# Kernel optimization log

Measured on AMD Instinct MI355X. Metric: run time of the kernel, lower is better.

## Reference

```python
import jax, jax.numpy as jnp
import numpy as np

C = 128  # in_dim

def _proj(x, w, b):
    # 1x1 conv: x [b,c,h,w], w [out,in], b [out] -> [b,out,h*w]
    bsz, c, h, wd = x.shape
    y = jnp.einsum('bchw,oc->bohw', x, w) + b[None, :, None, None]
    return y.reshape(bsz, -1, h * wd)

def setup_inputs() -> dict:
    key = jax.random.key(0)
    ks = jax.random.split(key, 7)
    x = jax.random.normal(ks[0], (16, C, 128, 128), dtype=jnp.float32)
    s = 1.0 / np.sqrt(C)
    qw = jax.random.normal(ks[1], (C, C), dtype=jnp.float32) * s
    kw = jax.random.normal(ks[2], (C, C), dtype=jnp.float32) * s
    vw = jax.random.normal(ks[3], (C, C), dtype=jnp.float32) * s
    qb = jax.random.normal(ks[4], (C,), dtype=jnp.float32) * 0.01
    kb = jax.random.normal(ks[5], (C,), dtype=jnp.float32) * 0.01
    vb = jax.random.normal(ks[6], (C,), dtype=jnp.float32) * 0.01
    return {'x': x, 'qw': qw, 'qb': qb, 'kw': kw, 'kb': kb, 'vw': vw, 'vb': vb}

def reference(x, qw, qb, kw, kb, vw, vb):
    x_s, x_t = jnp.split(x, 2, axis=0)
    b, c, h, w = x_s.shape
    q_s = _proj(x_s, qw, qb); q_t = _proj(x_t, qw, qb)   # [b,c,N]
    k_s = _proj(x_s, kw, kb); k_t = _proj(x_t, kw, kb)   # [b,c,N]
    v_s = _proj(x_s, vw, vb); v_t = _proj(x_t, vw, vb)   # [b,c,N]
    # channel cross-attentions: contract over spatial N -> [b,c,c]
    a_st = jax.nn.softmax(jnp.einsum('bcn,bdn->bcd', q_t, k_s), axis=-1)
    a_ts = jax.nn.softmax(jnp.einsum('bcn,bdn->bcd', q_s, k_t), axis=-1)
    att = jax.nn.softmax(jnp.einsum('bce,bde->bcd', a_st, a_ts), axis=-1)
    out_s = jnp.einsum('bcd,bdn->bcn', att, v_s).reshape(b, c, h, w)
    out_t = jnp.einsum('bcd,bdn->bcn', att, v_t).reshape(b, c, h, w)
    return jnp.concatenate((x_s + out_s, x_t + out_t), axis=0)
```

## Files before the change

### kernel.cpp

```cpp
#include <hip/hip_runtime.h>
#include <hip/hip_bf16.h>

#define CC 128
#define NSP 16384
#define NFULL (CC * NSP)

typedef float f32x4 __attribute__((ext_vector_type(4)));
typedef short s16x8 __attribute__((ext_vector_type(8)));
typedef unsigned int u32x4 __attribute__((ext_vector_type(4)));

__device__ __forceinline__ unsigned bf16rne(float f) {
  unsigned u = __float_as_uint(f);
  return ((u + 0x7FFFu + ((u >> 16) & 1u)) >> 16) & 0xFFFFu;
}

__device__ __forceinline__ uint2 packpair(float x0, float x1) {
  __hip_bfloat162 h2 = __float22bfloat162_rn(make_float2(x0, x1));
  unsigned hu = *reinterpret_cast<unsigned*>(&h2);
  float hf0 = __uint_as_float(hu << 16);
  float hf1 = __uint_as_float(hu & 0xFFFF0000u);
  __hip_bfloat162 l2 = __float22bfloat162_rn(make_float2(x0 - hf0, x1 - hf1));
  unsigned lu = *reinterpret_cast<unsigned*>(&l2);
  return make_uint2(hu, lu);
}

__global__ __launch_bounds__(256) void zerok(float* __restrict__ p, int n) {
  int i = blockIdx.x * 256 + threadIdx.x;
  if (i < n) p[i] = 0.f;
}

__global__ __launch_bounds__(256, 2) void k1_mfma(const float* __restrict__ x,
    float* __restrict__ Mdst, float* __restrict__ rs, float* __restrict__ rt,
    float* __restrict__ rspart, float* __restrict__ rtpart,
    int nst, int mode) {
  const int b = blockIdx.y;
  const int chunk = blockIdx.x;
  const int n0 = chunk * (nst * 64);
  const int t = threadIdx.x;
  const int w = t >> 6, l = t & 63;
  const int wr = w >> 1, wc = w & 1;
  const int lr = l & 15, lg = l >> 4;
  const int r0 = t >> 2;
  const int q = t & 3;
  __shared__ unsigned short Ahi[128 * 64];
  __shared__ unsigned short Alo[128 * 64];
  __shared__ unsigned short Bhi[128 * 64];
  __shared__ unsigned short Blo[128 * 64];
  const float* Xs = x + (size_t)b * NFULL;
  const float* Xt = x + (size_t)(b + 8) * NFULL;

  f32x4 acc[4][4];
#pragma unroll
  for (int a = 0; a < 4; ++a)
#pragma unroll
    for (int bb = 0; bb < 4; ++bb) acc[a][bb] = (f32x4){0.f, 0.f, 0.f, 0.f};
  float rtp[2] = {0.f, 0.f}, rsp[2] = {0.f, 0.f};

  for (int s = 0; s < nst; ++s) {
    const int nb = n0 + s * 64;
    __syncthreads();
#pragma unroll
    for (int p = 0; p < 2; ++p) {
      const int row = r0 + 64 * p;
      const float* At = Xt + (size_t)row * NSP + nb + q * 16;
      const float* Bs = Xs + (size_t)row * NSP + nb + q * 16;
      f32x4 av[4], bv[4];
#pragma unroll
      for (int i = 0; i < 4; ++i) av[i] = *(const f32x4*)(At + i * 4);
#pragma unroll
      for (int i = 0; i < 4; ++i) bv[i] = *(const f32x4*)(Bs + i * 4);
#pragma unroll
      for (int i = 0; i < 4; ++i) {
        rtp[p] += (av[i][0] + av[i][1]) + (av[i][2] + av[i][3]);
        rsp[p] += (bv[i][0] + bv[i][1]) + (bv[i][2] + bv[i][3]);
      }
      u32x4 h0, l0, h1, l1;
#pragma unroll
      for (int i = 0; i < 2; ++i) {
        uint2 r1 = packpair(av[i][0], av[i][1]);
        h0[2 * i] = r1.x; l0[2 * i] = r1.y;
        uint2 r2 = packpair(av[i][2], av[i][3]);
        h0[2 * i + 1] = r2.x; l0[2 * i + 1] = r2.y;
        uint2 r3 = packpair(av[2 + i][0], av[2 + i][1]);
        h1[2 * i] = r3.x; l1[2 * i] = r3.y;
        uint2 r4 = packpair(av[2 + i][2], av[2 + i][3]);
        h1[2 * i + 1] = r4.x; l1[2 * i + 1] = r4.y;
      }
      {
        int base = row * 128 + q * 32;
        int sw = (row & 7) << 4;
        *(u32x4*)((char*)Ahi + ((base) ^ sw)) = h0;
        *(u32x4*)((char*)Ahi + ((base + 16) ^ sw)) = h1;
        *(u32x4*)((char*)Alo + ((base) ^ sw)) = l0;
        *(u32x4*)((char*)Alo + ((base + 16) ^ sw)) = l1;
      }
#pragma unroll
      for (int i = 0; i < 2; ++i) {
        uint2 r1 = packpair(bv[i][0], bv[i][1]);
        h0[2 * i] = r1.x; l0[2 * i] = r1.y;
        uint2 r2 = packpair(bv[i][2], bv[i][3]);
        h0[2 * i + 1] = r2.x; l0[2 * i + 1] = r2.y;
        uint2 r3 = packpair(bv[2 + i][0], bv[2 + i][1]);
        h1[2 * i] = r3.x; l1[2 * i] = r3.y;
        uint2 r4 = packpair(bv[2 + i][2], bv[2 + i][3]);
        h1[2 * i + 1] = r4.x; l1[2 * i + 1] = r4.y;
      }
      {
        int base = row * 128 + q * 32;
        int sw = (row & 7) << 4;
        *(u32x4*)((char*)Bhi + ((base) ^ sw)) = h0;
        *(u32x4*)((char*)Bhi + ((base + 16) ^ sw)) = h1;
        *(u32x4*)((char*)Blo + ((base) ^ sw)) = l0;
        *(u32x4*)((char*)Blo + ((base + 16) ^ sw)) = l1;
      }
    }
    __syncthreads();
#pragma unroll
    for (int kk = 0; kk < 2; ++kk) {
      s16x8 ah[4], al[4], bh[4], bl[4];
#pragma unroll
      for (int a = 0; a < 4; ++a) {
        int row = wr * 64 + a * 16 + lr;
        int off = (row * 128 + kk * 64 + lg * 16) ^ ((row & 7) << 4);
        ah[a] = *(const s16x8*)((char*)Ahi + off);
        al[a] = *(const s16x8*)((char*)Alo + off);
      }
#pragma unroll
      for (int bb = 0; bb < 4; ++bb) {
        int row = wc * 64 + bb * 16 + lr;
        int off = (row * 128 + kk * 64 + lg * 16) ^ ((row & 7) << 4);
        bh[bb] = *(const s16x8*)((char*)Bhi + off);
        bl[bb] = *(const s16x8*)((char*)Blo + off);
      }
#pragma unroll
      for (int a = 0; a < 4; ++a)
#pragma unroll
        for (int bb = 0; bb < 4; ++bb) {
          acc[a][bb] = __builtin_amdgcn_mfma_f32_16x16x32_bf16(ah[a], bh[bb], acc[a][bb], 0, 0, 0);
          acc[a][bb] = __builtin_amdgcn_mfma_f32_16x16x32_bf16(ah[a], bl[bb], acc[a][bb], 0, 0, 0);
          acc[a][bb] = __builtin_amdgcn_mfma_f32_16x16x32_bf16(al[a], bh[bb], acc[a][bb], 0, 0, 0);
        }
    }
  }

#pragma unroll
  for (int p = 0; p < 2; ++p) {
    float vt = rtp[p];
    vt += __shfl_xor(vt, 1);
    vt += __shfl_xor(vt, 2);
    float vs = rsp[p];
    vs += __shfl_xor(vs, 1);
    vs += __shfl_xor(vs, 2);
    if (q == 0) {
      int row = r0 + 64 * p;
      if (mode == 0) {
        rtpart[((size_t)chunk * 8 + b) * CC + row] = vt;
        rspart[((size_t)chunk * 8 + b) * CC + row] = vs;
      } else {
        atomicAdd(&rt[b * CC + row], vt);
        atomicAdd(&rs[b * CC + row], vs);
      }
    }
  }

  const int rquad = lg << 2;
  if (mode == 0) {
    float* Mp = Mdst + ((size_t)chunk * 8 + b) * (CC * CC);
#pragma unroll
    for (int a = 0; a < 4; ++a)
#pragma unroll
      for (int bb = 0; bb < 4; ++bb)
#pragma unroll
        for (int r = 0; r < 4; ++r) {
          int i = wr * 64 + a * 16 + rquad + r;
          int j = wc * 64 + bb * 16 + lr;
          Mp[i * CC + j] = acc[a][bb][r];
        }
  } else {
    float* Mp = Mdst + (size_t)b * (CC * CC);
#pragma unroll
    for (int a = 0; a < 4; ++a)
#pragma unroll
      for (int bb = 0; bb < 4; ++bb)
#pragma unroll
        for (int r = 0; r < 4; ++r) {
          int i = wr * 64 + a * 16 + rquad + r;
          int j = wc * 64 + bb * 16 + lr;
          atomicAdd(&Mp[i * CC + j], acc[a][bb][r]);
        }
  }
}

__global__ __launch_bounds__(256) void k1_reduce(const float* __restrict__ Mpart,
    const float* __restrict__ rspart, const float* __restrict__ rtpart,
    float* __restrict__ M, float* __restrict__ rs, float* __restrict__ rt,
    int NB) {
  const int t = threadIdx.x;
  if (blockIdx.x < 128) {
    const int i4 = blockIdx.x * 256 + t;
    const int b = i4 >> 12;
    const int e = (i4 & 4095) * 4;
    f32x4 s = (f32x4){0.f, 0.f, 0.f, 0.f};
    for (int c = 0; c < NB; ++c) {
      f32x4 v = *(const f32x4*)(Mpart + ((size_t)c * 8 + b) * (CC * CC) + e);
      s += v;
    }
    *(f32x4*)(M + (size_t)b * CC * CC + e) = s;
  } else if (blockIdx.x == 128) {
    const int e = t * 4;
    f32x4 s = (f32x4){0.f, 0.f, 0.f, 0.f};
    for (int c = 0; c < NB; ++c) s += *(const f32x4*)(rtpart + (size_t)c * 1024 + e);
    *(f32x4*)(rt + e) = s;
  } else {
    const int e = t * 4;
    f32x4 s = (f32x4){0.f, 0.f, 0.f, 0.f};
    for (int c = 0; c < NB; ++c) s += *(const f32x4*)(rspart + (size_t)c * 1024 + e);
    *(f32x4*)(rs + e) = s;
  }
}

__global__ __launch_bounds__(256) void k2ab(const float* __restrict__ M,
    const float* __restrict__ qw, const float* __restrict__ kw,
    const float* __restrict__ qb, const float* __restrict__ kb,
    const float* __restrict__ rs, const float* __restrict__ rt,
    float* __restrict__ Ast, float* __restrict__ Ats) {
  const int b = blockIdx.y;
  const int c0 = blockIdx.x * 8;
  __shared__ float Big[128][132];
  __shared__ float Wq[8][128];
  __shared__ float T12[2][8][128];
  __shared__ float uvv[2][8];
  __shared__ float wv2[2][128];
  const int t = threadIdx.x;
  const float* Mb = M + (size_t)b * CC * CC;
#pragma unroll
  for (int p = 0; p < 16; ++p) {
    int f = p * 256 + t;
    int row = f >> 5, c4 = (f & 31) * 4;
    *(f32x4*)&Big[row][c4] = *(const f32x4*)(Mb + row * CC + c4);
  }
  { int row = t >> 5, c4 = (t & 31) * 4;
    *(f32x4*)&Wq[row][c4] = *(const f32x4*)(qw + (c0 + row) * CC + c4); }
  __syncthreads();
  if (t < 16) {
    int c = t & 7;
    const float* r = ((t < 8) ? rs : rt) + b * CC;
    float s = 0.f;
    for (int i = 0; i < CC; ++i) s += Wq[c][i] * r[i];
    uvv[(t < 8) ? 1 : 0][c] = s;
  }
  const int tr = t >> 5;
  const int L = t & 31;
  {
    float a1[4] = {0.f, 0.f, 0.f, 0.f}, a2[4] = {0.f, 0.f, 0.f, 0.f};
    for (int i = 0; i < CC; ++i) {
      float wq = Wq[tr][i];
#pragma unroll
      for (int j = 0; j < 4; ++j) a1[j] += wq * Big[i][L + 32 * j];
    }
    for (int i4 = 0; i4 < 32; ++i4) {
      f32x4 wq4 = *(const f32x4*)&Wq[tr][i4 * 4];
#pragma unroll
      for (int j = 0; j < 4; ++j) {
        f32x4 m4 = *(const f32x4*)&Big[L + 32 * j][i4 * 4];
        a2[j] += wq4[0]*m4[0] + wq4[1]*m4[1] + wq4[2]*m4[2] + wq4[3]*m4[3];
      }
    }
#pragma unroll
    for (int j = 0; j < 4; ++j) {
      T12[0][tr][L + 32 * j] = a1[j];
      T12[1][tr][L + 32 * j] = a2[j];
    }
  }
  __syncthreads();
#pragma unroll
  for (int p = 0; p < 16; ++p) {
    int f = p * 256 + t;
    int row = f >> 5, c4 = (f & 31) * 4;
    *(f32x4*)&Big[row][c4] = *(const f32x4*)(kw + row * CC + c4);
  }
  __syncthreads();
  {
    int d = t & 127, wh = t >> 7;
    const float* r = (wh ? rt : rs) + b * CC;
    float s = 0.f;
    for (int i4 = 0; i4 < 32; ++i4) {
      f32x4 w4 = *(const f32x4*)&Big[d][i4 * 4];
      s += w4[0]*r[i4*4] + w4[1]*r[i4*4+1] + w4[2]*r[i4*4+2] + w4[3]*r[i4*4+3];
    }
    wv2[wh][d] = s;
  }
  __syncthreads();
  const int c = c0 + tr;
  const float bqc = qb[c];
#pragma unroll 1
  for (int which = 0; which < 2; ++which) {
    float g[4];
#pragma unroll
    for (int j = 0; j < 4; ++j) {
      int d = L + 32 * j;
      g[j] = uvv[which][tr] * kb[d] + bqc * wv2[which][d] + 16384.f * bqc * kb[d];
    }
    for (int j4 = 0; j4 < 32; ++j4) {
      f32x4 tv4 = *(const f32x4*)&T12[which][tr][j4 * 4];
#pragma unroll
      for (int j = 0; j < 4; ++j) {
        f32x4 w4 = *(const f32x4*)&Big[L + 32 * j][j4 * 4];
        g[j] += tv4[0]*w4[0] + tv4[1]*w4[1] + tv4[2]*w4[2] + tv4[3]*w4[3];
      }
    }
    float m = fmaxf(fmaxf(g[0], g[1]), fmaxf(g[2], g[3]));
#pragma unroll
    for (int off = 1; off < 32; off <<= 1) m = fmaxf(m, __shfl_xor(m, off));
    float s = 0.f;
#pragma unroll
    for (int j = 0; j < 4; ++j) { g[j] = expf(g[j] - m); s += g[j]; }
#pragma unroll
    for (int off = 1; off < 32; off <<= 1) s += __shfl_xor(s, off);
    const float inv = 1.f / s;
    float* A = (which ? Ats : Ast) + (size_t)b * CC * CC + (size_t)c * CC;
#pragma unroll
    for (int j = 0; j < 4; ++j) A[L + 32 * j] = g[j] * inv;
  }
}

__global__ __launch_bounds__(256) void k2cd(const float* __restrict__ Ast,
    const float* __restrict__ Ats, const float* __restrict__ vw,
    const float* __restrict__ vb, unsigned short* __restrict__ Pbf,
    float* __restrict__ c0v) {
  const int b = blockIdx.y;
  const int c0 = blockIdx.x * 8;
  __shared__ float Big[128][132];
  __shared__ float Tl[8][128];
  __shared__ float Al[8][128];
  const int t = threadIdx.x;
  const float* Bb = Ats + (size_t)b * CC * CC;
  const float* Tb = Ast + (size_t)b * CC * CC;
#pragma unroll
  for (int p = 0; p < 16; ++p) {
    int f = p * 256 + t;
    int row = f >> 5, c4 = (f & 31) * 4;
    *(f32x4*)&Big[row][c4] = *(const f32x4*)(Bb + row * CC + c4);
  }
  { int row = t >> 5, c4 = (t & 31) * 4;
    *(f32x4*)&Tl[row][c4] = *(const f32x4*)(Tb + (c0 + row) * CC + c4); }
  __syncthreads();
  const int tr = t >> 5;
  const int L = t & 31;
  {
    float g[4] = {0.f, 0.f, 0.f, 0.f};
    for (int e4 = 0; e4 < 32; ++e4) {
      f32x4 tv4 = *(const f32x4*)&Tl[tr][e4 * 4];
#pragma unroll
      for (int j = 0; j < 4; ++j) {
        f32x4 a4 = *(const f32x4*)&Big[L + 32 * j][e4 * 4];
        g[j] += tv4[0]*a4[0] + tv4[1]*a4[1] + tv4[2]*a4[2] + tv4[3]*a4[3];
      }
    }
    float m = fmaxf(fmaxf(g[0], g[1]), fmaxf(g[2], g[3]));
#pragma unroll
    for (int off = 1; off < 32; off <<= 1) m = fmaxf(m, __shfl_xor(m, off));
    float s = 0.f;
#pragma unroll
    for (int j = 0; j < 4; ++j) { g[j] = expf(g[j] - m); s += g[j]; }
#pragma unroll
    for (int off = 1; off < 32; off <<= 1) s += __shfl_xor(s, off);
    const float inv = 1.f / s;
#pragma unroll
    for (int j = 0; j < 4; ++j) Al[tr][L + 32 * j] = g[j] * inv;
  }
  __syncthreads();
#pragma unroll
  for (int p = 0; p < 16; ++p) {
    int f = p * 256 + t;
    int row = f >> 5, c4 = (f & 31) * 4;
    *(f32x4*)&Big[row][c4] = *(const f32x4*)(vw + row * CC + c4);
  }
  __syncthreads();
  float p4[4] = {0.f, 0.f, 0.f, 0.f};
  for (int d = 0; d < CC; ++d) {
    float av = Al[tr][d];
#pragma unroll
    for (int j = 0; j < 4; ++j) p4[j] += av * Big[d][L + 32 * j];
  }
  float csum = 0.f;
#pragma unroll
  for (int j = 0; j < 4; ++j) csum += Al[tr][L + 32 * j] * vb[L + 32 * j];
#pragma unroll
  for (int off = 1; off < 32; off <<= 1) csum += __shfl_xor(csum, off);
  const int c = c0 + tr;
  if ((c & 31) == L) p4[c >> 5] += 1.0f;
  unsigned short* Pp = Pbf + (size_t)b * CC * CC + (size_t)c * CC;
#pragma unroll
  for (int j = 0; j < 4; ++j) Pp[L + 32 * j] = (unsigned short)bf16rne(p4[j]);
  if (L == 0) c0v[b * CC + c] = csum;
}

__global__ __launch_bounds__(256, 2) void k3_mfma(const float* __restrict__ x,
    const unsigned short* __restrict__ Pbf, const float* __restrict__ c0v,
    float* __restrict__ out) {
  const int im = blockIdx.y;
  const int pb = im & 7;
  const int n0 = blockIdx.x * 256;
  const float* X = x + (size_t)im * NFULL;
  float* O = out + (size_t)im * NFULL;
  __shared__ unsigned short XT[256 * 128];
  __shared__ float c0l[128];
  const int t = threadIdx.x;
  if (t < 128) c0l[t] = c0v[pb * CC + t];
#pragma unroll
  for (int p = 0; p < 16; ++p) {
    int d0 = 2 * (t >> 4) + 32 * (p & 3);
    int n4 = (t & 15) * 4 + 64 * (p >> 2);
    f32x4 x0 = *(const f32x4*)(X + (size_t)d0 * NSP + n0 + n4);
    f32x4 x1 = *(const f32x4*)(X + (size_t)(d0 + 1) * NSP + n0 + n4);
#pragma unroll
    for (int i = 0; i < 4; ++i) {
      int n = n4 + i;
      __hip_bfloat162 h2 = __float22bfloat162_rn(make_float2(x0[i], x1[i]));
      unsigned pk = *reinterpret_cast<unsigned*>(&h2);
      int off = (n * 256 + d0 * 2) ^ (((n >> 2) & 15) << 4);
      *(unsigned*)((char*)XT + off) = pk;
    }
  }
  __syncthreads();

  const int w = t >> 6, l = t & 63;
  const int ln = l & 15, lg = l >> 4;
#pragma unroll
  for (int h = 0; h < 2; ++h) {
    const unsigned short* Pg = Pbf + (size_t)pb * (CC * CC)
                             + (size_t)(h * 64 + ln) * CC + lg * 8;
    s16x8 Af[4][4];
#pragma unroll
    for (int a = 0; a < 4; ++a)
#pragma unroll
      for (int kk = 0; kk < 4; ++kk)
        Af[a][kk] = *(const s16x8*)(Pg + a * 16 * CC + kk * 32);
#pragma unroll
    for (int sub = 0; sub < 4; ++sub) {
      int row = sub * 64 + w * 16 + ln;
      int sw = ((row >> 2) & 15) << 4;
      s16x8 bf[4];
#pragma unroll
      for (int kk = 0; kk < 4; ++kk)
        bf[kk] = *(const s16x8*)((char*)XT + ((row * 256 + kk * 64 + lg * 16) ^ sw));
      f32x4 acc[4];
#pragma unroll
      for (int a = 0; a < 4; ++a) acc[a] = (f32x4){0.f, 0.f, 0.f, 0.f};
#pragma unroll
      for (int kk = 0; kk < 4; ++kk)
#pragma unroll
        for (int a = 0; a < 4; ++a)
          acc[a] = __builtin_amdgcn_mfma_f32_16x16x32_bf16(Af[a][kk], bf[kk], acc[a], 0, 0, 0);
      int n = n0 + sub * 64 + w * 16 + ln;
#pragma unroll
      for (int a = 0; a < 4; ++a)
#pragma unroll
        for (int r = 0; r < 4; ++r) {
          int c = h * 64 + a * 16 + lg * 4 + r;
          __builtin_nontemporal_store(acc[a][r] + c0l[c], O + (size_t)c * NSP + n);
        }
    }
  }
}

extern "C" void kernel_launch(void* const* d_in, const int* in_sizes, int n_in,
                              void* d_out, int out_size, void* d_ws, size_t ws_size,
                              hipStream_t stream) {
  (void)in_sizes; (void)n_in; (void)out_size;
  const float* x  = (const float*)d_in[0];
  const float* qw = (const float*)d_in[1];
  const float* qb = (const float*)d_in[2];
  const float* kw = (const float*)d_in[3];
  const float* kb = (const float*)d_in[4];
  const float* vw = (const float*)d_in[5];
  const float* vb = (const float*)d_in[6];
  float* out = (float*)d_out;
  float* ws = (float*)d_ws;
  float* M   = ws;
  float* rs  = M + 131072;
  float* rt  = rs + 1024;
  float* AST = rt + 1024;
  float* ATS = AST + 131072;
  unsigned short* Pbf = (unsigned short*)(ATS + 131072);
  float* c0v = ATS + 131072 + 65536;
  float* Mpart = c0v + 1024;
  const size_t base_floats = (size_t)(Mpart - ws);

  int NB, mode;
  if (ws_size >= (base_floats + (size_t)64 * (131072 + 2048)) * 4) { NB = 64; mode = 0; }
  else if (ws_size >= (base_floats + (size_t)32 * (131072 + 2048)) * 4) { NB = 32; mode = 0; }
  else { NB = 32; mode = 1; }
  const int nst = (16384 / NB) / 64;
  float* rtpart = Mpart + (size_t)NB * 131072;
  float* rspart = rtpart + (size_t)NB * 1024;

  if (mode == 1) zerok<<<(133120 + 255) / 256, 256, 0, stream>>>(M, 133120);
  k1_mfma<<<dim3(NB, 8), 256, 0, stream>>>(x, mode ? M : Mpart, rs, rt,
                                           rspart, rtpart, nst, mode);
  if (mode == 0)
    k1_reduce<<<130, 256, 0, stream>>>(Mpart, rspart, rtpart, M, rs, rt, NB);
  k2ab<<<dim3(16, 8), 256, 0, stream>>>(M, qw, kw, qb, kb, rs, rt, AST, ATS);
  k2cd<<<dim3(16, 8), 256, 0, stream>>>(AST, ATS, vw, vb, Pbf, c0v);
  k3_mfma<<<dim3(64, 16), 256, 0, stream>>>(x, Pbf, c0v, out);
}
```

Measured before the change: 145.6 us.

## Double-buffer raw fp32 tiles via direct global-to-LDS loads and split at fragment read

Result: no change. 147.2 us (+1.1%).

```diff
diff --git a/kernel.cpp b/kernel.cpp
--- a/kernel.cpp
+++ b/kernel.cpp
@@ -8,6 +8,10 @@
 typedef float f32x4 __attribute__((ext_vector_type(4)));
 typedef short s16x8 __attribute__((ext_vector_type(8)));
 typedef unsigned int u32x4 __attribute__((ext_vector_type(4)));
+
+#define GLOAD16(g, l) __builtin_amdgcn_global_load_lds( \
+    (const __attribute__((address_space(1))) void*)(g), \
+    (__attribute__((address_space(3))) void*)(l), 16, 0, 0)
 
 __device__ __forceinline__ unsigned bf16rne(float f) {
   unsigned u = __float_as_uint(f);
@@ -35,130 +39,111 @@
     int nst, int mode) {
   const int b = blockIdx.y;
   const int chunk = blockIdx.x;
-  const int n0 = chunk * (nst * 64);
+  const int n0 = chunk * (nst * 32);
   const int t = threadIdx.x;
   const int w = t >> 6, l = t & 63;
   const int wr = w >> 1, wc = w & 1;
   const int lr = l & 15, lg = l >> 4;
-  const int r0 = t >> 2;
-  const int q = t & 3;
-  __shared__ unsigned short Ahi[128 * 64];
-  __shared__ unsigned short Alo[128 * 64];
-  __shared__ unsigned short Bhi[128 * 64];
-  __shared__ unsigned short Blo[128 * 64];
+  __shared__ __align__(16) char LB[2][2][128 * 128];
   const float* Xs = x + (size_t)b * NFULL;
   const float* Xt = x + (size_t)(b + 8) * NFULL;
+  const int srow0 = w * 32 + (l >> 3);
+  const int sn16x = (l & 7);
 
   f32x4 acc[4][4];
 #pragma unroll
   for (int a = 0; a < 4; ++a)
 #pragma unroll
     for (int bb = 0; bb < 4; ++bb) acc[a][bb] = (f32x4){0.f, 0.f, 0.f, 0.f};
-  float rtp[2] = {0.f, 0.f}, rsp[2] = {0.f, 0.f};
+  float rtp[4] = {0.f, 0.f, 0.f, 0.f};
+  float rsp[4] = {0.f, 0.f, 0.f, 0.f};
+
+  {
+#pragma unroll
+    for (int i = 0; i < 4; ++i) {
+      int row = srow0 + i * 8;
+      int n16 = sn16x ^ (row & 7);
+      GLOAD16(Xt + (size_t)row * NSP + n0 + n16 * 4, &LB[0][0][(w * 32 + i * 8) * 128]);
+      GLOAD16(Xs + (size_t)row * NSP + n0 + n16 * 4, &LB[0][1][(w * 32 + i * 8) * 128]);
+    }
+  }
 
   for (int s = 0; s < nst; ++s) {
-    const int nb = n0 + s * 64;
+    const int cur = s & 1;
     __syncthreads();
-#pragma unroll
-    for (int p = 0; p < 2; ++p) {
-      const int row = r0 + 64 * p;
-      const float* At = Xt + (size_t)row * NSP + nb + q * 16;
-      const float* Bs = Xs + (size_t)row * NSP + nb + q * 16;
-      f32x4 av[4], bv[4];
-#pragma unroll
-      for (int i = 0; i < 4; ++i) av[i] = *(const f32x4*)(At + i * 4);
-#pragma unroll
-      for (int i = 0; i < 4; ++i) bv[i] = *(const f32x4*)(Bs + i * 4);
+    if (s + 1 < nst) {
+      const int nb = n0 + (s + 1) * 32;
 #pragma unroll
       for (int i = 0; i < 4; ++i) {
-        rtp[p] += (av[i][0] + av[i][1]) + (av[i][2] + av[i][3]);
-        rsp[p] += (bv[i][0] + bv[i][1]) + (bv[i][2] + bv[i][3]);
-      }
-      u32x4 h0, l0, h1, l1;
-#pragma unroll
-      for (int i = 0; i < 2; ++i) {
-        uint2 r1 = packpair(av[i][0], av[i][1]);
-        h0[2 * i] = r1.x; l0[2 * i] = r1.y;
-        uint2 r2 = packpair(av[i][2], av[i][3]);
-        h0[2 * i + 1] = r2.x; l0[2 * i + 1] = r2.y;
-        uint2 r3 = packpair(av[2 + i][0], av[2 + i][1]);
-        h1[2 * i] = r3.x; l1[2 * i] = r3.y;
-        uint2 r4 = packpair(av[2 + i][2], av[2 + i][3]);
-        h1[2 * i + 1] = r4.x; l1[2 * i + 1] = r4.y;
-      }
-      {
-        int base = row * 128 + q * 32;
-        int sw = (row & 7) << 4;
-        *(u32x4*)((char*)Ahi + ((base) ^ sw)) = h0;
-        *(u32x4*)((char*)Ahi + ((base + 16) ^ sw)) = h1;
-        *(u32x4*)((char*)Alo + ((base) ^ sw)) = l0;
-        *(u32x4*)((char*)Alo + ((base + 16) ^ sw)) = l1;
-      }
-#pragma unroll
-      for (int i = 0; i < 2; ++i) {
-        uint2 r1 = packpair(bv[i][0], bv[i][1]);
-        h0[2 * i] = r1.x; l0[2 * i] = r1.y;
-        uint2 r2 = packpair(bv[i][2], bv[i][3]);
-        h0[2 * i + 1] = r2.x; l0[2 * i + 1] = r2.y;
-        uint2 r3 = packpair(bv[2 + i][0], bv[2 + i][1]);
-        h1[2 * i] = r3.x; l1[2 * i] = r3.y;
-        uint2 r4 = packpair(bv[2 + i][2], bv[2 + i][3]);
-        h1[2 * i + 1] = r4.x; l1[2 * i + 1] = r4.y;
-      }
-      {
-        int base = row * 128 + q * 32;
-        int sw = (row & 7) << 4;
-        *(u32x4*)((char*)Bhi + ((base) ^ sw)) = h0;
-        *(u32x4*)((char*)Bhi + ((base + 16) ^ sw)) = h1;
-        *(u32x4*)((char*)Blo + ((base) ^ sw)) = l0;
-        *(u32x4*)((char*)Blo + ((base + 16) ^ sw)) = l1;
-      }
-    }
-    __syncthreads();
-#pragma unroll
-    for (int kk = 0; kk < 2; ++kk) {
-      s16x8 ah[4], al[4], bh[4], bl[4];
-#pragma unroll
-      for (int a = 0; a < 4; ++a) {
-        int row = wr * 64 + a * 16 + lr;
-        int off = (row * 128 + kk * 64 + lg * 16) ^ ((row & 7) << 4);
-        ah[a] = *(const s16x8*)((char*)Ahi + off);
-        al[a] = *(const s16x8*)((char*)Alo + off);
-      }
+        int row = srow0 + i * 8;
+        int n16 = sn16x ^ (row & 7);
+        GLOAD16(Xt + (size_t)row * NSP + nb + n16 * 4, &LB[cur ^ 1][0][(w * 32 + i * 8) * 128]);
+        GLOAD16(Xs + (size_t)row * NSP + nb + n16 * 4, &LB[cur ^ 1][1][(w * 32 + i * 8) * 128]);
+      }
+    }
+    const char* A = &LB[cur][0][0];
+    const char* B = &LB[cur][1][0];
+    s16x8 ah[4], al[4], bh[4], bl[4];
+#pragma unroll
+    for (int a = 0; a < 4; ++a) {
+      int row = wr * 64 + a * 16 + lr;
+      int base = row * 128, sw = row & 7;
+      f32x4 f0 = *(const f32x4*)(A + base + (((lg * 2) ^ sw) << 4));
+      f32x4 f1 = *(const f32x4*)(A + base + (((lg * 2 + 1) ^ sw) << 4));
+      rtp[a] += ((f0[0] + f0[1]) + (f0[2] + f0[3])) + ((f1[0] + f1[1]) + (f1[2] + f1[3]));
+      uint2 p0 = packpair(f0[0], f0[1]);
+      uint2 p1 = packpair(f0[2], f0[3]);
+      uint2 p2 = packpair(f1[0], f1[1]);
+      uint2 p3 = packpair(f1[2], f1[3]);
+      u32x4 H = {p0.x, p1.x, p2.x, p3.x};
+      u32x4 L = {p0.y, p1.y, p2.y, p3.y};
+      ah[a] = __builtin_bit_cast(s16x8, H);
+      al[a] = __builtin_bit_cast(s16x8, L);
+    }
+#pragma unroll
+    for (int bb = 0; bb < 4; ++bb) {
+      int row = wc * 64 + bb * 16 + lr;
+      int base = row * 128, sw = row & 7;
+      f32x4 f0 = *(const f32x4*)(B + base + (((lg * 2) ^ sw) << 4));
+      f32x4 f1 = *(const f32x4*)(B + base + (((lg * 2 + 1) ^ sw) << 4));
+      rsp[bb] += ((f0[0] + f0[1]) + (f0[2] + f0[3])) + ((f1[0] + f1[1]) + (f1[2] + f1[3]));
+      uint2 p0 = packpair(f0[0], f0[1]);
+      uint2 p1 = packpair(f0[2], f0[3]);
+      uint2 p2 = packpair(f1[0], f1[1]);
+      uint2 p3 = packpair(f1[2], f1[3]);
+      u32x4 H = {p0.x, p1.x, p2.x, p3.x};
+      u32x4 L = {p0.y, p1.y, p2.y, p3.y};
+      bh[bb] = __builtin_bit_cast(s16x8, H);
+      bl[bb] = __builtin_bit_cast(s16x8, L);
+    }
+#pragma unroll
+    for (int a = 0; a < 4; ++a)
 #pragma unroll
       for (int bb = 0; bb < 4; ++bb) {
-        int row = wc * 64 + bb * 16 + lr;
-        int off = (row * 128 + kk * 64 + lg * 16) ^ ((row & 7) << 4);
-        bh[bb] = *(const s16x8*)((char*)Bhi + off);
-        bl[bb] = *(const s16x8*)((char*)Blo + off);
-      }
-#pragma unroll
-      for (int a = 0; a < 4; ++a)
-#pragma unroll
-        for (int bb = 0; bb < 4; ++bb) {
-          acc[a][bb] = __builtin_amdgcn_mfma_f32_16x16x32_bf16(ah[a], bh[bb], acc[a][bb], 0, 0, 0);
-          acc[a][bb] = __builtin_amdgcn_mfma_f32_16x16x32_bf16(ah[a], bl[bb], acc[a][bb], 0, 0, 0);
-          acc[a][bb] = __builtin_amdgcn_mfma_f32_16x16x32_bf16(al[a], bh[bb], acc[a][bb], 0, 0, 0);
-        }
-    }
-  }
-
-#pragma unroll
-  for (int p = 0; p < 2; ++p) {
-    float vt = rtp[p];
-    vt += __shfl_xor(vt, 1);
-    vt += __shfl_xor(vt, 2);
-    float vs = rsp[p];
-    vs += __shfl_xor(vs, 1);
-    vs += __shfl_xor(vs, 2);
-    if (q == 0) {
-      int row = r0 + 64 * p;
-      if (mode == 0) {
-        rtpart[((size_t)chunk * 8 + b) * CC + row] = vt;
-        rspart[((size_t)chunk * 8 + b) * CC + row] = vs;
-      } else {
-        atomicAdd(&rt[b * CC + row], vt);
-        atomicAdd(&rs[b * CC + row], vs);
+        acc[a][bb] = __builtin_amdgcn_mfma_f32_16x16x32_bf16(ah[a], bh[bb], acc[a][bb], 0, 0, 0);
+        acc[a][bb] = __builtin_amdgcn_mfma_f32_16x16x32_bf16(ah[a], bl[bb], acc[a][bb], 0, 0, 0);
+        acc[a][bb] = __builtin_amdgcn_mfma_f32_16x16x32_bf16(al[a], bh[bb], acc[a][bb], 0, 0, 0);
+      }
+  }
+
+#pragma unroll
+  for (int a = 0; a < 4; ++a) {
+    float vt = rtp[a];
+    vt += __shfl_xor(vt, 16);
+    vt += __shfl_xor(vt, 32);
+    float vs = rsp[a];
+    vs += __shfl_xor(vs, 16);
+    vs += __shfl_xor(vs, 32);
+    if (l < 16) {
+      if (wc == 0) {
+        int row = wr * 64 + a * 16 + l;
+        if (mode == 0) rtpart[((size_t)chunk * 8 + b) * CC + row] = vt;
+        else atomicAdd(&rt[b * CC + row], vt);
+      }
+      if (wr == 0) {
+        int row = wc * 64 + a * 16 + l;
+        if (mode == 0) rspart[((size_t)chunk * 8 + b) * CC + row] = vs;
+        else atomicAdd(&rs[b * CC + row], vs);
       }
     }
   }
@@ -492,7 +477,7 @@
   if (ws_size >= (base_floats + (size_t)64 * (131072 + 2048)) * 4) { NB = 64; mode = 0; }
   else if (ws_size >= (base_floats + (size_t)32 * (131072 + 2048)) * 4) { NB = 32; mode = 0; }
   else { NB = 32; mode = 1; }
-  const int nst = (16384 / NB) / 64;
+  const int nst = (16384 / NB) / 32;
   float* rtpart = Mpart + (size_t)NB * 131072;
   float* rspart = rtpart + (size_t)NB * 1024;
 
```
